# Performance work log

Hardware: AMD Instinct MI355X
Metric: run time of the kernel (lower is better)

Reference implementation:

```python
import jax, jax.numpy as jnp
import numpy as np

D = 256      # input channels
DK = 64      # key/query/value channels
BS, W, H = 8, 64, 64


def setup_inputs() -> dict:
    key = jax.random.key(0)
    k1, k2, k3, k4 = jax.random.split(key, 4)
    v = jax.random.normal(k1, (BS, D, W, H), dtype=jnp.float32)
    # conv1x1 weights collapse to plain matrices over the channel dim
    Wqkv = jax.random.normal(k2, (3 * DK, D), dtype=jnp.float32) * 0.02
    Wout = jax.random.normal(k3, (D, DK), dtype=jnp.float32) * 0.02
    gamma = jax.random.normal(k4, (1,), dtype=jnp.float32)  # original inits to 0; nonzero for a non-degenerate baseline
    return {"v": v, "Wqkv": Wqkv, "Wout": Wout, "gamma": gamma}


def reference(v, Wqkv, Wout, gamma):
    bs, c, w, h = v.shape
    n = w * h
    d_k = Wout.shape[1]
    x = v.reshape(bs, c, n)                      # (b, c, n)
    qkv = jnp.einsum('oc,bcn->bon', Wqkv, x)      # 1x1 conv == channel matmul
    q = qkv[:, :d_k]                              # (b, dk, n)
    k = qkv[:, d_k:2 * d_k]
    val = qkv[:, 2 * d_k:]
    s = jnp.einsum('bdi,bdj->bij', q, k)          # (b, n, n) = query^T key
    beta = jax.nn.softmax(s, axis=2)              # exp(s - logsumexp(s, axis=2))
    y = jnp.einsum('bdi,bij->bdj', val, beta)     # bmm(value, beta)
    o = jnp.einsum('od,bdn->bon', Wout, y) * gamma[0] + x
    return o.reshape(bs, c, w, h)
```

## Files before the change

kernel.cpp:

```cpp
#include <hip/hip_runtime.h>

typedef unsigned short ushort_t;
typedef __bf16 bf16x8 __attribute__((ext_vector_type(8)));
typedef short short4v __attribute__((ext_vector_type(4)));
typedef float f32x4 __attribute__((ext_vector_type(4)));
typedef unsigned int uint4v __attribute__((ext_vector_type(4)));
typedef unsigned int uint2v __attribute__((ext_vector_type(2)));

#define NTOK 4096
#define DMODEL 256
#define DK 64
#define BS 8
#define LN2INV 1.44269504088896f

__device__ __forceinline__ ushort_t f2bf(float f) {
  unsigned u = __builtin_bit_cast(unsigned, f);
  u += 0x7fffu + ((u >> 16) & 1u);
  return (ushort_t)(u >> 16);
}
__device__ __forceinline__ float bf2f(ushort_t s) {
  return __builtin_bit_cast(float, ((unsigned)s) << 16);
}
__device__ __forceinline__ bf16x8 lds_frag(const ushort_t* p) {
  return __builtin_bit_cast(bf16x8, *(const uint4v*)p);
}
__device__ __forceinline__ bf16x8 ldg8(const ushort_t* p) {
  return __builtin_bit_cast(bf16x8, *(const uint4v*)p);
}
__device__ __forceinline__ short4v lo8(uint4v v) {
  uint2v t; t.x = v.x; t.y = v.y;
  return __builtin_bit_cast(short4v, t);
}
__device__ __forceinline__ short4v hi8(uint4v v) {
  uint2v t; t.x = v.z; t.y = v.w;
  return __builtin_bit_cast(short4v, t);
}
__device__ __forceinline__ float fexp2(float x) {
#if __has_builtin(__builtin_amdgcn_exp2f)
  return __builtin_amdgcn_exp2f(x);
#else
  return exp2f(x);
#endif
}
__device__ __forceinline__ unsigned bfpack(float x, float y) {
  return __builtin_amdgcn_perm(__builtin_bit_cast(unsigned, y),
                               __builtin_bit_cast(unsigned, x), 0x07060302u);
}
__device__ __forceinline__ f32x4 mfma16(short4v a, short4v b, f32x4 c) {
#if defined(__HIP_DEVICE_COMPILE__)
#if __has_builtin(__builtin_amdgcn_mfma_f32_16x16x16bf16_1k)
  return __builtin_amdgcn_mfma_f32_16x16x16bf16_1k(a, b, c, 0, 0, 0);
#else
  typedef __bf16 bf16x4 __attribute__((ext_vector_type(4)));
  return __builtin_amdgcn_mfma_f32_16x16x16_bf16(__builtin_bit_cast(bf16x4, a),
                                                 __builtin_bit_cast(bf16x4, b), c, 0, 0, 0);
#endif
#else
  (void)a; (void)b;
  return c;
#endif
}

typedef __attribute__((address_space(3))) unsigned int lds_u32;
typedef const __attribute__((address_space(1))) unsigned int glob_u32;
__device__ __forceinline__ void gll16(const void* g, void* l) {
#if defined(__HIP_DEVICE_COMPILE__)
  __builtin_amdgcn_global_load_lds((glob_u32*)g, (lds_u32*)l, 16, 0, 0);
#else
  (void)g; (void)l;
#endif
}

__global__ __launch_bounds__(256) void k_convert(const float* __restrict__ Wqkv,
                                                 const float* __restrict__ Wout,
                                                 ushort_t* __restrict__ Wb,
                                                 ushort_t* __restrict__ Woutb) {
  int i = blockIdx.x * 256 + threadIdx.x;
  if (i < 3 * DK * DMODEL) {
    float w = Wqkv[i];
    if (i < DK * DMODEL) w *= LN2INV;
    Wb[i] = f2bf(w);
  } else {
    int j = i - 3 * DK * DMODEL;
    Woutb[j] = f2bf(Wout[j]);
  }
}

__global__ __launch_bounds__(256) void k_qkv(const float* __restrict__ x,
                                             const ushort_t* __restrict__ W,
                                             ushort_t* __restrict__ QT,
                                             ushort_t* __restrict__ KT,
                                             ushort_t* __restrict__ Vf) {
  const int b = blockIdx.y;
  const int n0 = blockIdx.x * 64;
  const int tid = threadIdx.x;
  const int lane = tid & 63, wv = tid >> 6;
  const int quad = lane >> 4, l15 = lane & 15;
  __shared__ __align__(16) ushort_t lx[64 * 264];
  __shared__ __align__(16) ushort_t t[64 * 72];

  const float* xb = x + (size_t)b * DMODEL * NTOK;

#pragma unroll 1
  for (int cc = 0; cc < 4; cc++) {
    const int c0chunk = cc * 64;
#pragma unroll
    for (int kr = 0; kr < 2; kr++) {
      int s = tid + 256 * kr;
      int c = s >> 3, ns = (s & 7) * 8;
      const float* src = xb + (size_t)(c0chunk + c) * NTOK + n0 + ns;
      f32x4 a = *(const f32x4*)src;
      f32x4 bq = *(const f32x4*)(src + 4);
      uint4v o;
      o.x = (unsigned)f2bf(a[0]) | ((unsigned)f2bf(a[1]) << 16);
      o.y = (unsigned)f2bf(a[2]) | ((unsigned)f2bf(a[3]) << 16);
      o.z = (unsigned)f2bf(bq[0]) | ((unsigned)f2bf(bq[1]) << 16);
      o.w = (unsigned)f2bf(bq[2]) | ((unsigned)f2bf(bq[3]) << 16);
      *(uint4v*)(t + c * 72 + ns) = o;
    }
    __syncthreads();
#pragma unroll
    for (int kr = 0; kr < 2; kr++) {
      int s = tid + 256 * kr;
      int n = s >> 3, cs = (s & 7) * 8;
      unsigned e0 = t[(cs + 0) * 72 + n], e1 = t[(cs + 1) * 72 + n];
      unsigned e2 = t[(cs + 2) * 72 + n], e3 = t[(cs + 3) * 72 + n];
      unsigned e4 = t[(cs + 4) * 72 + n], e5 = t[(cs + 5) * 72 + n];
      unsigned e6 = t[(cs + 6) * 72 + n], e7 = t[(cs + 7) * 72 + n];
      uint4v o;
      o.x = e0 | (e1 << 16); o.y = e2 | (e3 << 16);
      o.z = e4 | (e5 << 16); o.w = e6 | (e7 << 16);
      *(uint4v*)(lx + n * 264 + c0chunk + cs) = o;
    }
    __syncthreads();
  }

  f32x4 acc[3][4];
  const f32x4 zero4 = {0.f, 0.f, 0.f, 0.f};
#pragma unroll
  for (int i = 0; i < 3; i++)
#pragma unroll
    for (int j = 0; j < 4; j++) acc[i][j] = zero4;

#pragma unroll
  for (int c0 = 0; c0 < DMODEL; c0 += 32) {
    bf16x8 aw[3];
#pragma unroll
    for (int mt = 0; mt < 3; mt++)
      aw[mt] = ldg8(W + (wv * 48 + mt * 16 + l15) * DMODEL + c0 + quad * 8);
    bf16x8 bb[4];
#pragma unroll
    for (int nt = 0; nt < 4; nt++)
      bb[nt] = lds_frag(lx + (nt * 16 + l15) * 264 + c0 + quad * 8);
#pragma unroll
    for (int mt = 0; mt < 3; mt++)
#pragma unroll
      for (int nt = 0; nt < 4; nt++)
        acc[mt][nt] = __builtin_amdgcn_mfma_f32_16x16x32_bf16(aw[mt], bb[nt], acc[mt][nt], 0, 0, 0);
  }

#pragma unroll
  for (int mt = 0; mt < 3; mt++) {
    int o = wv * 48 + mt * 16 + quad * 4;
#pragma unroll
    for (int nt = 0; nt < 4; nt++) {
      int n = n0 + nt * 16 + l15;
      f32x4 v4 = acc[mt][nt];
      if (o < 128) {
        ushort_t* dst = (o < 64) ? (QT + ((size_t)b * NTOK + n) * DK + o)
                                 : (KT + ((size_t)b * NTOK + n) * DK + (o - 64));
        uint2v ww;
        ww.x = (unsigned)f2bf(v4[0]) | ((unsigned)f2bf(v4[1]) << 16);
        ww.y = (unsigned)f2bf(v4[2]) | ((unsigned)f2bf(v4[3]) << 16);
        *(uint2v*)dst = ww;
      } else {
        int dbase = o - 128;
        size_t tbase = ((((size_t)b * 64 + (n0 >> 6)) * 4 + nt) * 2 + (dbase >> 5)) * 512;
        ushort_t* vp = Vf + tbase + ((l15 >> 2) << 7) + ((dbase & 15) << 3) +
                       (((dbase >> 4) & 1) << 2) + (l15 & 3);
#pragma unroll
        for (int r = 0; r < 4; r++) vp[r << 3] = f2bf(v4[r]);
      }
    }
  }
}

__global__ __launch_bounds__(512, 4) void k_rsum(const ushort_t* __restrict__ QT,
                                                 const ushort_t* __restrict__ KT,
                                                 float* __restrict__ Rr) {
  const int id = blockIdx.x;
  const int b = id & 7;
  const int i0 = (id >> 3) * 64;
  const int tid = threadIdx.x;
  const int lane = tid & 63, wv = tid >> 6;
  const int quad = lane >> 4, l15 = lane & 15;
  __shared__ __align__(16) float partial[8 * 64];
  const ushort_t* QTb = QT + ((size_t)b * NTOK + i0) * DK;
  const ushort_t* KTb = KT + ((size_t)b * NTOK + wv * 512) * DK;

  bf16x8 aq0[4], aq1[4];
#pragma unroll
  for (int isub = 0; isub < 4; isub++) {
    const ushort_t* qp = QTb + (size_t)(isub * 16 + l15) * DK + quad * 8;
    aq0[isub] = ldg8(qp);
    aq1[isub] = ldg8(qp + 32);
  }

  f32x4 racc[4];
  const f32x4 zero4 = {0.f, 0.f, 0.f, 0.f};
#pragma unroll
  for (int isub = 0; isub < 4; isub++) racc[isub] = zero4;

#pragma unroll 1
  for (int ph = 0; ph < 8; ph++) {
    const ushort_t* kb_base = KTb + (size_t)ph * 64 * DK;
    bf16x8 kb0[4], kb1[4];
#pragma unroll
    for (int nt = 0; nt < 4; nt++) {
      const ushort_t* kp = kb_base + (size_t)(nt * 16 + l15) * DK + quad * 8;
      kb0[nt] = ldg8(kp);
      kb1[nt] = ldg8(kp + 32);
    }
#pragma unroll
    for (int isub = 0; isub < 4; isub++)
#pragma unroll
      for (int nt = 0; nt < 4; nt++) {
        f32x4 s4 = __builtin_amdgcn_mfma_f32_16x16x32_bf16(aq0[isub], kb0[nt], zero4, 0, 0, 0);
        s4 = __builtin_amdgcn_mfma_f32_16x16x32_bf16(aq1[isub], kb1[nt], s4, 0, 0, 0);
        racc[isub][0] += fexp2(s4[0]);
        racc[isub][1] += fexp2(s4[1]);
        racc[isub][2] += fexp2(s4[2]);
        racc[isub][3] += fexp2(s4[3]);
      }
  }

#pragma unroll
  for (int isub = 0; isub < 4; isub++)
#pragma unroll
    for (int r = 0; r < 4; r++) {
      float v = racc[isub][r];
      v += __shfl_xor(v, 1);
      v += __shfl_xor(v, 2);
      v += __shfl_xor(v, 4);
      v += __shfl_xor(v, 8);
      racc[isub][r] = v;
    }
  if (l15 == 0) {
#pragma unroll
    for (int isub = 0; isub < 4; isub++)
      *(f32x4*)(partial + wv * 64 + isub * 16 + quad * 4) = racc[isub];
  }
  __syncthreads();
  if (tid < 64) {
    float s = 0.f;
#pragma unroll
    for (int w = 0; w < 8; w++) s += partial[w * 64 + tid];
    Rr[(size_t)b * NTOK + i0 + tid] = -__log2f(s);
  }
}

__global__ __launch_bounds__(256, 4) void k_pv(const ushort_t* __restrict__ QT,
                                               const ushort_t* __restrict__ KT,
                                               const ushort_t* __restrict__ Vf,
                                               const float* __restrict__ Rr,
                                               ushort_t* __restrict__ Yp) {
  const int id = blockIdx.x;
  const int b = id & 7;
  const int rest = id >> 3;
  const int j0 = (rest & 63) * 64;
  const int ih = rest >> 6;
  const int tid = threadIdx.x;
  const int lane = tid & 63, wv = tid >> 6;
  const int quad = lane >> 4, l15 = lane & 15;

  __shared__ __align__(16) ushort_t pool[20480];
  float* lrtab = (float*)pool;
  ushort_t* wbuf = pool + 4096 + wv * 4096;
  float* rbuf = (float*)pool;
  ushort_t* pbuf = pool + 8704;

  const ushort_t* KTb = KT + ((size_t)b * NTOK + j0) * DK;
  const ushort_t* QTb = QT + ((size_t)b * NTOK + ih * 2048) * DK;
  const ushort_t* Vfb = Vf + ((size_t)b * 64 + ih * 32) * 4096;
  const float* Rrb = Rr + (size_t)b * NTOK + ih * 2048;

  const int qrow = (wv * 16 + l15) * DK + quad * 8;
  const int vfo = wv * 1024 + lane * 8;

  gll16(QTb + qrow,       wbuf);
  gll16(QTb + qrow + 32,  wbuf + 512);
  gll16(Vfb + vfo,        wbuf + 1024);
  gll16(Vfb + vfo + 512,  wbuf + 1536);

  {
    f32x4 r0 = *(const f32x4*)(Rrb + tid * 8);
    f32x4 r1 = *(const f32x4*)(Rrb + tid * 8 + 4);
    *(f32x4*)(lrtab + tid * 8) = r0;
    *(f32x4*)(lrtab + tid * 8 + 4) = r1;
  }

  bf16x8 kb0[4], kb1[4];
#pragma unroll
  for (int nt = 0; nt < 4; nt++) {
    const ushort_t* kp = KTb + (size_t)(nt * 16 + l15) * DK + quad * 8;
    kb0[nt] = ldg8(kp);
    kb1[nt] = ldg8(kp + 32);
  }

  __syncthreads();

  f32x4 yt[4][4];
  const f32x4 zero4 = {0.f, 0.f, 0.f, 0.f};
#pragma unroll
  for (int i = 0; i < 4; i++)
#pragma unroll
    for (int j = 0; j < 4; j++) yt[i][j] = zero4;

#pragma unroll 1
  for (int it = 0; it < 32; it++) {
    const int cb = it & 1, nb = cb ^ 1;
    const int tpre = (it + 1 < 32) ? it + 1 : 31;
    {
      const ushort_t* qp = QTb + (size_t)tpre * 64 * DK + qrow;
      const ushort_t* vp = Vfb + (size_t)tpre * 4096 + vfo;
      ushort_t* nbuf = wbuf + nb * 2048;
      gll16(qp,       nbuf);
      gll16(qp + 32,  nbuf + 512);
      gll16(vp,       nbuf + 1024);
      gll16(vp + 512, nbuf + 1536);
    }
    asm volatile("s_waitcnt vmcnt(4)" ::: "memory");
    __builtin_amdgcn_sched_barrier(0);
    const ushort_t* cbuf = wbuf + cb * 2048;
    bf16x8 a0 = lds_frag(cbuf + lane * 8);
    bf16x8 a1 = lds_frag(cbuf + 512 + lane * 8);
    uint4v vv0 = *(const uint4v*)(cbuf + 1024 + lane * 8);
    uint4v vv1 = *(const uint4v*)(cbuf + 1536 + lane * 8);
    f32x4 lrv = *(const f32x4*)(lrtab + it * 64 + wv * 16 + quad * 4);
    short4v vf0 = lo8(vv0), vf1 = hi8(vv0), vf2 = lo8(vv1), vf3 = hi8(vv1);
#pragma unroll
    for (int nt = 0; nt < 4; nt++) {
      f32x4 s4 = __builtin_amdgcn_mfma_f32_16x16x32_bf16(a0, kb0[nt], lrv, 0, 0, 0);
      s4 = __builtin_amdgcn_mfma_f32_16x16x32_bf16(a1, kb1[nt], s4, 0, 0, 0);
      uint2v wp;
      wp.x = bfpack(fexp2(s4[0]), fexp2(s4[1]));
      wp.y = bfpack(fexp2(s4[2]), fexp2(s4[3]));
      short4v wf = __builtin_bit_cast(short4v, wp);
      yt[nt][0] = mfma16(wf, vf0, yt[nt][0]);
      yt[nt][1] = mfma16(wf, vf1, yt[nt][1]);
      yt[nt][2] = mfma16(wf, vf2, yt[nt][2]);
      yt[nt][3] = mfma16(wf, vf3, yt[nt][3]);
    }
  }

  asm volatile("s_waitcnt vmcnt(0)" ::: "memory");
  __syncthreads();

  if (wv == 0) {
#pragma unroll
    for (int nt = 0; nt < 4; nt++)
#pragma unroll
      for (int dsub = 0; dsub < 4; dsub++)
        *(f32x4*)(rbuf + (dsub * 16 + l15) * 68 + nt * 16 + quad * 4) = yt[nt][dsub];
  }
  __syncthreads();
  if (wv == 1) {
#pragma unroll
    for (int nt = 0; nt < 4; nt++)
#pragma unroll
      for (int dsub = 0; dsub < 4; dsub++) {
        float* p = rbuf + (dsub * 16 + l15) * 68 + nt * 16 + quad * 4;
        *(f32x4*)p = *(const f32x4*)p + yt[nt][dsub];
      }
  }
  __syncthreads();
  if (wv == 2) {
#pragma unroll
    for (int nt = 0; nt < 4; nt++)
#pragma unroll
      for (int dsub = 0; dsub < 4; dsub++) {
        float* p = rbuf + (dsub * 16 + l15) * 68 + nt * 16 + quad * 4;
        *(f32x4*)p = *(const f32x4*)p + yt[nt][dsub];
      }
  }
  __syncthreads();
  if (wv == 3) {
#pragma unroll
    for (int nt = 0; nt < 4; nt++)
#pragma unroll
      for (int dsub = 0; dsub < 4; dsub++) {
        const float* p = rbuf + (dsub * 16 + l15) * 68 + nt * 16 + quad * 4;
        f32x4 v4 = *(const f32x4*)p + yt[nt][dsub];
#pragma unroll
        for (int r = 0; r < 4; r++)
          pbuf[(nt * 16 + quad * 4 + r) * 72 + dsub * 16 + l15] = f2bf(v4[r]);
      }
  }
  __syncthreads();

  ushort_t* Ypb = Yp + ((size_t)(ih * 8 + b) * NTOK + j0) * DK;
#pragma unroll
  for (int kr = 0; kr < 2; kr++) {
    int s = tid + 256 * kr;
    int row = s >> 3, cc = (s & 7) * 8;
    *(uint4v*)(Ypb + (size_t)row * DK + cc) = *(const uint4v*)(pbuf + row * 72 + cc);
  }
}

__global__ __launch_bounds__(256) void k_out(const ushort_t* __restrict__ Yp,
                                             const ushort_t* __restrict__ Wout,
                                             const float* __restrict__ gammap,
                                             const float* __restrict__ x,
                                             float* __restrict__ outp) {
  const int id = blockIdx.x;
  const int b = id & 7;
  const int n0 = (id >> 3) * 64;
  const int tid = threadIdx.x;
  const int lane = tid & 63, wv = tid >> 6;
  const int quad = lane >> 4, l15 = lane & 15;
  __shared__ __align__(16) ushort_t pbuf[64 * 72];

  const ushort_t* Y0 = Yp + ((size_t)b * NTOK + n0) * DK;
  const ushort_t* Y1 = Yp + ((size_t)(8 + b) * NTOK + n0) * DK;
#pragma unroll
  for (int kr = 0; kr < 2; kr++) {
    int s = tid + 256 * kr;
    int row = s >> 3, c8 = (s & 7) * 8;
    uint4v ua = *(const uint4v*)(Y0 + (size_t)row * DK + c8);
    uint4v ub = *(const uint4v*)(Y1 + (size_t)row * DK + c8);
    uint4v oc;
    unsigned* pa = (unsigned*)&ua;
    unsigned* pb = (unsigned*)&ub;
    unsigned* po = (unsigned*)&oc;
#pragma unroll
    for (int w = 0; w < 4; w++) {
      float lo = bf2f((ushort_t)(pa[w] & 0xffff)) + bf2f((ushort_t)(pb[w] & 0xffff));
      float hi = bf2f((ushort_t)(pa[w] >> 16)) + bf2f((ushort_t)(pb[w] >> 16));
      po[w] = bfpack(lo, hi);
    }
    *(uint4v*)(pbuf + row * 72 + c8) = oc;
  }
  __syncthreads();

  const f32x4 zero4 = {0.f, 0.f, 0.f, 0.f};
  bf16x8 yb0[4], yb1[4];
#pragma unroll
  for (int nt = 0; nt < 4; nt++) {
    yb0[nt] = lds_frag(pbuf + (nt * 16 + l15) * 72 + quad * 8);
    yb1[nt] = lds_frag(pbuf + (nt * 16 + l15) * 72 + 32 + quad * 8);
  }
  f32x4 oacc[4][4];
#pragma unroll
  for (int m = 0; m < 4; m++)
#pragma unroll
    for (int nt = 0; nt < 4; nt++) oacc[m][nt] = zero4;
#pragma unroll
  for (int m = 0; m < 4; m++) {
    int c = (wv * 4 + m) * 16 + l15;
    bf16x8 aw0 = __builtin_bit_cast(bf16x8, *(const uint4v*)(Wout + c * DK + quad * 8));
    bf16x8 aw1 = __builtin_bit_cast(bf16x8, *(const uint4v*)(Wout + c * DK + 32 + quad * 8));
#pragma unroll
    for (int nt = 0; nt < 4; nt++) {
      oacc[m][nt] = __builtin_amdgcn_mfma_f32_16x16x32_bf16(aw0, yb0[nt], oacc[m][nt], 0, 0, 0);
      oacc[m][nt] = __builtin_amdgcn_mfma_f32_16x16x32_bf16(aw1, yb1[nt], oacc[m][nt], 0, 0, 0);
    }
  }
  float g = gammap[0];
  const float* xb = x + (size_t)b * DMODEL * NTOK;
  float* ob = outp + (size_t)b * DMODEL * NTOK;
#pragma unroll
  for (int m = 0; m < 4; m++) {
    int cbase = (wv * 4 + m) * 16 + quad * 4;
#pragma unroll
    for (int nt = 0; nt < 4; nt++) {
      int n = n0 + nt * 16 + l15;
#pragma unroll
      for (int r = 0; r < 4; r++) {
        size_t idx = (size_t)(cbase + r) * NTOK + n;
        ob[idx] = oacc[m][nt][r] * g + xb[idx];
      }
    }
  }
}

extern "C" void kernel_launch(void* const* d_in, const int* in_sizes, int n_in,
                              void* d_out, int out_size, void* d_ws, size_t ws_size,
                              hipStream_t stream) {
  const float* v = (const float*)d_in[0];
  const float* Wqkv = (const float*)d_in[1];
  const float* Wout = (const float*)d_in[2];
  const float* gamma = (const float*)d_in[3];
  float* outp = (float*)d_out;

  ushort_t* QT = (ushort_t*)d_ws;
  ushort_t* KT = QT + (size_t)BS * NTOK * DK;
  ushort_t* Vf = KT + (size_t)BS * NTOK * DK;
  ushort_t* Wb = Vf + (size_t)BS * DK * NTOK;
  ushort_t* Woutb = Wb + 3 * DK * DMODEL;
  float* Rr = (float*)(Woutb + DMODEL * DK);
  ushort_t* Yp = (ushort_t*)(Rr + (size_t)BS * NTOK);

  k_convert<<<dim3(256), 256, 0, stream>>>(Wqkv, Wout, Wb, Woutb);
  k_qkv<<<dim3(64, BS), 256, 0, stream>>>(v, Wb, QT, KT, Vf);
  k_rsum<<<dim3(512), 512, 0, stream>>>(QT, KT, Rr);
  k_pv<<<dim3(1024), 256, 0, stream>>>(QT, KT, Vf, Rr, Yp);
  k_out<<<dim3(512), 256, 0, stream>>>(Yp, Woutb, gamma, v, outp);
}
```

Measured before the change: 201.9 us.

## Stage QKV projection outputs through LDS and load V directly in PV loop

The projection kernel now writes its Q/K/V tiles into shared memory first and then copies them to global memory with coalesced 16-byte stores, replacing scattered 8-byte and 2-byte global writes. In the PV kernel, V fragments are loaded straight from global into registers at the top of each iteration instead of being staged through the LDS double buffer. This halves that kernel's shared-memory footprint, which could allow more resident blocks. The trade-off is two extra barriers in the projection kernel, and V loads in the PV loop that are issued in the same iteration they are used, with no prefetch ahead.

```diff
diff --git a/kernel.cpp b/kernel.cpp
--- a/kernel.cpp
+++ b/kernel.cpp
@@ -159,29 +159,47 @@
         acc[mt][nt] = __builtin_amdgcn_mfma_f32_16x16x32_bf16(aw[mt], bb[nt], acc[mt][nt], 0, 0, 0);
   }
 
+  __syncthreads();
+  ushort_t* qk_t = lx;
+  ushort_t* v_t = lx + 128 * 68;
 #pragma unroll
   for (int mt = 0; mt < 3; mt++) {
     int o = wv * 48 + mt * 16 + quad * 4;
 #pragma unroll
     for (int nt = 0; nt < 4; nt++) {
-      int n = n0 + nt * 16 + l15;
+      int nl = nt * 16 + l15;
       f32x4 v4 = acc[mt][nt];
       if (o < 128) {
-        ushort_t* dst = (o < 64) ? (QT + ((size_t)b * NTOK + n) * DK + o)
-                                 : (KT + ((size_t)b * NTOK + n) * DK + (o - 64));
         uint2v ww;
         ww.x = (unsigned)f2bf(v4[0]) | ((unsigned)f2bf(v4[1]) << 16);
         ww.y = (unsigned)f2bf(v4[2]) | ((unsigned)f2bf(v4[3]) << 16);
-        *(uint2v*)dst = ww;
+        int row = (o < 64) ? nl : 64 + nl;
+        *(uint2v*)(qk_t + row * 68 + (o & 63)) = ww;
       } else {
         int dbase = o - 128;
-        size_t tbase = ((((size_t)b * 64 + (n0 >> 6)) * 4 + nt) * 2 + (dbase >> 5)) * 512;
-        ushort_t* vp = Vf + tbase + ((l15 >> 2) << 7) + ((dbase & 15) << 3) +
-                       (((dbase >> 4) & 1) << 2) + (l15 & 3);
-#pragma unroll
-        for (int r = 0; r < 4; r++) vp[r << 3] = f2bf(v4[r]);
+        int idx = (nt * 2 + (dbase >> 5)) * 512 + ((l15 >> 2) << 7) +
+                  ((dbase & 15) << 3) + (((dbase >> 4) & 1) << 2) + (l15 & 3);
+#pragma unroll
+        for (int r = 0; r < 4; r++) v_t[idx + (r << 3)] = f2bf(v4[r]);
       }
     }
+  }
+  __syncthreads();
+  {
+    ushort_t* QTb = QT + ((size_t)b * NTOK + n0) * DK;
+    ushort_t* KTb = KT + ((size_t)b * NTOK + n0) * DK;
+#pragma unroll
+    for (int k = 0; k < 4; k++) {
+      int s = tid + 256 * k;
+      int row = s >> 3, seg = (s & 7) * 8;
+      uint4v val = *(const uint4v*)(qk_t + row * 68 + seg);
+      ushort_t* dst = (row < 64) ? (QTb + (size_t)row * DK + seg)
+                                 : (KTb + (size_t)(row - 64) * DK + seg);
+      *(uint4v*)dst = val;
+    }
+    ushort_t* Vtile = Vf + ((size_t)b * 64 + (n0 >> 6)) * 4096;
+    *(uint4v*)(Vtile + tid * 8) = *(const uint4v*)(v_t + tid * 8);
+    *(uint4v*)(Vtile + 2048 + tid * 8) = *(const uint4v*)(v_t + 2048 + tid * 8);
   }
 }
 
@@ -273,9 +291,9 @@
   const int lane = tid & 63, wv = tid >> 6;
   const int quad = lane >> 4, l15 = lane & 15;
 
-  __shared__ __align__(16) ushort_t pool[20480];
+  __shared__ __align__(16) ushort_t pool[13312];
   float* lrtab = (float*)pool;
-  ushort_t* wbuf = pool + 4096 + wv * 4096;
+  ushort_t* wbuf = pool + 4096 + wv * 2048;
   float* rbuf = (float*)pool;
   ushort_t* pbuf = pool + 8704;
 
@@ -287,10 +305,8 @@
   const int qrow = (wv * 16 + l15) * DK + quad * 8;
   const int vfo = wv * 1024 + lane * 8;
 
-  gll16(QTb + qrow,       wbuf);
-  gll16(QTb + qrow + 32,  wbuf + 512);
-  gll16(Vfb + vfo,        wbuf + 1024);
-  gll16(Vfb + vfo + 512,  wbuf + 1536);
+  gll16(QTb + qrow,      wbuf);
+  gll16(QTb + qrow + 32, wbuf + 512);
 
   {
     f32x4 r0 = *(const f32x4*)(Rrb + tid * 8);
@@ -319,24 +335,23 @@
 #pragma unroll 1
   for (int it = 0; it < 32; it++) {
     const int cb = it & 1, nb = cb ^ 1;
-    const int tpre = (it + 1 < 32) ? it + 1 : 31;
+    const ushort_t* vp = Vfb + (size_t)it * 4096 + vfo;
+    uint4v vv0 = *(const uint4v*)vp;
+    uint4v vv1 = *(const uint4v*)(vp + 512);
+    f32x4 lrv = *(const f32x4*)(lrtab + it * 64 + wv * 16 + quad * 4);
+    asm volatile("" ::: "memory");
     {
+      const int tpre = (it + 1 < 32) ? it + 1 : 31;
       const ushort_t* qp = QTb + (size_t)tpre * 64 * DK + qrow;
-      const ushort_t* vp = Vfb + (size_t)tpre * 4096 + vfo;
-      ushort_t* nbuf = wbuf + nb * 2048;
-      gll16(qp,       nbuf);
-      gll16(qp + 32,  nbuf + 512);
-      gll16(vp,       nbuf + 1024);
-      gll16(vp + 512, nbuf + 1536);
-    }
-    asm volatile("s_waitcnt vmcnt(4)" ::: "memory");
+      ushort_t* nbuf = wbuf + nb * 1024;
+      gll16(qp,      nbuf);
+      gll16(qp + 32, nbuf + 512);
+    }
+    asm volatile("s_waitcnt vmcnt(2)" ::: "memory");
     __builtin_amdgcn_sched_barrier(0);
-    const ushort_t* cbuf = wbuf + cb * 2048;
+    const ushort_t* cbuf = wbuf + cb * 1024;
     bf16x8 a0 = lds_frag(cbuf + lane * 8);
     bf16x8 a1 = lds_frag(cbuf + 512 + lane * 8);
-    uint4v vv0 = *(const uint4v*)(cbuf + 1024 + lane * 8);
-    uint4v vv1 = *(const uint4v*)(cbuf + 1536 + lane * 8);
-    f32x4 lrv = *(const f32x4*)(lrtab + it * 64 + wv * 16 + quad * 4);
     short4v vf0 = lo8(vv0), vf1 = hi8(vv0), vf2 = lo8(vv1), vf3 = hi8(vv1);
 #pragma unroll
     for (int nt = 0; nt < 4; nt++) {
```

Result: slower. 215.4 us (+6.7%).
